# Performance work log

Measured on AMD Instinct MI355X. Metric: run time of the kernel, lower is better.

The kernel has to match this reference:

```python
import jax, jax.numpy as jnp
import numpy as np

S, B, V, E, H = 64, 32, 32000, 512, 1024


def gru_cell(x, h, Wih, Whh, bih, bhh):
    # PyTorch GRU cell math. x: [B, in], h: [B, H]
    gi = x @ Wih.T + bih          # [B, 3H]
    gh = h @ Whh.T + bhh          # [B, 3H]
    ir, iz, inn = jnp.split(gi, 3, axis=-1)
    hr, hz, hn = jnp.split(gh, 3, axis=-1)
    r = jax.nn.sigmoid(ir + hr)
    z = jax.nn.sigmoid(iz + hz)
    n = jnp.tanh(inn + r * hn)
    return (1.0 - z) * n + z * h


def run_gru(xs, h0, Wih, Whh, bih, bhh):
    def step(h, x):
        h = gru_cell(x, h, Wih, Whh, bih, bhh)
        return h, h
    _, hs = jax.lax.scan(step, h0, xs)
    return hs  # [S, B, H]


def setup_inputs():
    key = jax.random.key(0)
    ks = jax.random.split(key, 24)
    n = lambda k, shp, s=0.05: (jax.random.normal(k, shp, jnp.float32) * s)
    inp = {
        "input_seq": jax.random.randint(ks[0], (S, B), 0, V),
        "target_seq": jax.random.randint(ks[1], (S, B), 0, V),
        "emb": n(ks[2], (V, E)),
        # bidirectional encoder GRU (forward / backward directions)
        "enc_Wih_f": n(ks[3], (3 * H, E)), "enc_Whh_f": n(ks[4], (3 * H, H)),
        "enc_bih_f": n(ks[5], (3 * H,)),  "enc_bhh_f": n(ks[6], (3 * H,)),
        "enc_Wih_b": n(ks[7], (3 * H, E)), "enc_Whh_b": n(ks[8], (3 * H, H)),
        "enc_bih_b": n(ks[9], (3 * H,)),  "enc_bhh_b": n(ks[10], (3 * H,)),
        "encoder_init": n(ks[11], (2, H), 0.1),
        # decoder GRU: input = token(E) + glimpse(2H) + last_output(E)
        "dec_Wih": n(ks[12], (3 * H, 2 * E + 2 * H)), "dec_Whh": n(ks[13], (3 * H, H)),
        "dec_bih": n(ks[14], (3 * H,)), "dec_bhh": n(ks[15], (3 * H,)),
        "dec_init_h": n(ks[16], (H,), 0.1),
        "dec_init_out": n(ks[17], (E,), 0.1),
        "attn_W1": n(ks[18], (H, 3 * H)),  # Linear(3H -> H, bias=False)
        "attn_W2": n(ks[19], (1, H)),      # Linear(H -> 1, bias=False)
        "out_W": n(ks[20], (V, H)), "out_b": n(ks[21], (V,)),
    }
    return inp


def reference(input_seq, target_seq, emb,
              enc_Wih_f, enc_Whh_f, enc_bih_f, enc_bhh_f,
              enc_Wih_b, enc_Whh_b, enc_bih_b, enc_bhh_b, encoder_init,
              dec_Wih, dec_Whh, dec_bih, dec_bhh, dec_init_h, dec_init_out,
              attn_W1, attn_W2, out_W, out_b):
    x = emb[input_seq]            # [S, B, E]
    tgt = emb[target_seq]         # [S, B, E]
    bsz = x.shape[1]

    # bidirectional encoder
    h0f = jnp.broadcast_to(encoder_init[0], (bsz, H))
    h0b = jnp.broadcast_to(encoder_init[1], (bsz, H))
    fwd = run_gru(x, h0f, enc_Wih_f, enc_Whh_f, enc_bih_f, enc_bhh_f)
    bwd = run_gru(x[::-1], h0b, enc_Wih_b, enc_Whh_b, enc_bih_b, enc_bhh_b)[::-1]
    enc = jnp.concatenate([fwd, bwd], axis=-1)  # [S, B, 2H]

    def step(carry, inp_t):
        h, last_out = carry                      # [B,H], [B,E]
        tok, tg = inp_t                          # [B,E], [B,E]
        hexp = jnp.broadcast_to(h[None], (S, bsz, H))
        a = jnp.concatenate([enc, hexp], axis=-1)            # [S, B, 3H]
        scores = jnp.tanh(a @ attn_W1.T) @ attn_W2.T          # [S, B, 1]
        # NOTE: original uses nn.Softmax(dim=1) on [S,B,1] -> softmax over BATCH dim
        w = jax.nn.softmax(scores, axis=1)
        glimpse = (enc * w).sum(axis=0)                       # [B, 2H]
        dec_in = jnp.concatenate([tok, glimpse, last_out], axis=-1)
        h = gru_cell(dec_in, h, dec_Wih, dec_Whh, dec_bih, dec_bhh)
        probs = jax.nn.softmax(h @ out_W.T + out_b, axis=1)   # [B, V]
        return (h, tg), probs

    h0 = jnp.broadcast_to(dec_init_h, (bsz, H))
    o0 = jnp.broadcast_to(dec_init_out, (bsz, E))
    _, outs = jax.lax.scan(step, (h0, o0), (x, tgt))
    return outs  # [S, B, V]
```

## Files before the change

### kernel.cpp

```cpp
#include <hip/hip_runtime.h>
#include <hip/hip_bf16.h>

#define S_ 64
#define B_ 32
#define V_ 32000
#define E_ 512
#define H_ 1024
#define H3_ 3072

typedef __hip_bfloat16 bf16;
typedef __attribute__((ext_vector_type(8))) short s8v;
typedef __attribute__((ext_vector_type(4))) float f4;
typedef unsigned long long ull;

__device__ __forceinline__ float b2f(bf16 x){ return __bfloat162float(x); }
__device__ __forceinline__ bf16  f2b(float x){ return __float2bfloat16(x); }
__device__ __forceinline__ float bfu2f(unsigned short u){
  union { unsigned u; float f; } c; c.u = ((unsigned)u) << 16; return c.f;
}
#define MFMA16(a,b,c) __builtin_amdgcn_mfma_f32_16x16x32_bf16((a),(b),(c),0,0,0)

__device__ __forceinline__ float fsigmoid(float x){ return 1.f/(1.f + __expf(-x)); }
__device__ __forceinline__ float ftanh(float x){ float e2 = __expf(2.f*x); return 1.f - 2.f/(e2 + 1.f); }

__device__ __forceinline__ void gl16(const bf16* g, bf16* l){
  __builtin_amdgcn_global_load_lds((const __attribute__((address_space(1))) void*)g,
                                   (__attribute__((address_space(3))) void*)l, 16, 0, 0);
}

__device__ __forceinline__ void cast8(const float* __restrict__ s, bf16* __restrict__ d, int i){
  f4 a = *((const f4*)s + (size_t)i*2);
  f4 b = *((const f4*)s + (size_t)i*2 + 1);
  union { s8v v; bf16 h[8]; } o;
  #pragma unroll
  for (int k=0;k<4;k++){ o.h[k]=f2b(a[k]); o.h[4+k]=f2b(b[k]); }
  *((s8v*)d + i) = o.v;
}

__global__ __launch_bounds__(256) void prep_all_k(
  const float* __restrict__ emb, const int* __restrict__ iseq, const int* __restrict__ tseq,
  const float* __restrict__ dino,
  const float* __restrict__ wihf, const float* __restrict__ wihb,
  const float* __restrict__ whhf, const float* __restrict__ whhb,
  const float* __restrict__ whhd, const float* __restrict__ w1,
  const float* __restrict__ wihd, const float* __restrict__ outw,
  const float* __restrict__ einit, const float* __restrict__ bihf,
  const float* __restrict__ bihb, const float* __restrict__ dinh,
  bf16* __restrict__ x_b, bf16* __restrict__ lo_b,
  bf16* __restrict__ wihf_b, bf16* __restrict__ wihb_b,
  bf16* __restrict__ whhf_b, bf16* __restrict__ whhb_b,
  bf16* __restrict__ whhd_b, bf16* __restrict__ w1_b,
  bf16* __restrict__ wihd_b, bf16* __restrict__ outw_b,
  bf16* __restrict__ henc_b, float* __restrict__ hfE, float* __restrict__ bias_fb,
  bf16* __restrict__ hdb, float* __restrict__ hfD)
{
  const int task = blockIdx.y;
  const int stride = gridDim.x*256;
  const int i00 = blockIdx.x*256 + threadIdx.x;
  if (task < 8){
    const float* s; bf16* d; int n8;
    switch(task){
      case 0: s=wihf; d=wihf_b; n8=196608; break;
      case 1: s=wihb; d=wihb_b; n8=196608; break;
      case 2: s=whhf; d=whhf_b; n8=393216; break;
      case 3: s=whhb; d=whhb_b; n8=393216; break;
      case 4: s=whhd; d=whhd_b; n8=393216; break;
      case 5: s=w1;   d=w1_b;   n8=393216; break;
      case 6: s=wihd; d=wihd_b; n8=1179648; break;
      default: s=outw; d=outw_b; n8=4096000; break;
    }
    for (int i = i00; i < n8; i += stride) cast8(s, d, i);
  } else if (task == 8 || task == 9){
    for (int i = i00; i < 131072; i += stride){
      int row = i>>6, e8 = i&63;
      const float* src; bf16* d;
      if (task == 8){ src = emb + (size_t)iseq[row]*E_; d = x_b; }
      else {
        int t = row>>5, b = row&31;
        src = (t == 0) ? dino : (emb + (size_t)tseq[(t-1)*B_ + b]*E_);
        d = lo_b;
      }
      f4 a = *((const f4*)src + e8*2);
      f4 b = *((const f4*)src + e8*2 + 1);
      union { s8v v; bf16 h[8]; } o;
      #pragma unroll
      for (int k=0;k<4;k++){ o.h[k]=f2b(a[k]); o.h[4+k]=f2b(b[k]); }
      *((s8v*)d + i) = o.v;
    }
  } else if (task == 10){
    for (int i = i00; i < 8192; i += stride){
      int base = i*8;
      int dir = base>>15, rem = base&32767, col = rem&1023;
      const float* sp = einit + dir*H_ + col;
      f4 a = *(const f4*)sp, b = *(const f4*)(sp+4);
      union { s8v v; bf16 h[8]; } o;
      #pragma unroll
      for (int k=0;k<4;k++){ o.h[k]=f2b(a[k]); o.h[4+k]=f2b(b[k]); }
      *(s8v*)(henc_b + dir*32768 + rem) = o.v;
      *(f4*)(hfE + dir*32768 + rem) = a;
      *(f4*)(hfE + dir*32768 + rem + 4) = b;
      if (i < 6144) bias_fb[i] = (i < 3072) ? bihf[i] : bihb[i-3072];
    }
  } else {
    for (int i = i00; i < 4096; i += stride){
      int base = i*8;
      int col = base&1023;
      const float* sp = dinh + col;
      f4 a = *(const f4*)sp, b = *(const f4*)(sp+4);
      union { s8v v; bf16 h[8]; } o;
      #pragma unroll
      for (int k=0;k<4;k++){ o.h[k]=f2b(a[k]); o.h[4+k]=f2b(b[k]); }
      *(s8v*)(hdb + base) = o.v;
      *(f4*)(hfD + base) = a;
      *(f4*)(hfD + base + 4) = b;
    }
  }
}

template<int WB16>
__global__ __launch_bounds__(256) void gemm_bt(const bf16* __restrict__ A, int lda,
                                               const bf16* __restrict__ B, int ldb,
                                               const float* __restrict__ bias,
                                               void* __restrict__ Cp, int ldc, int K)
{
  __shared__ bf16 a_sm[128][32];
  __shared__ bf16 b_sm[128][32];
  const int tid = threadIdx.x;
  const int m0 = blockIdx.y*128, n0 = blockIdx.x*128;
  const int w = tid>>6, l = tid&63;
  const int wm = w>>1, wn = w&1;
  f4 acc[4][4];
  #pragma unroll
  for (int i=0;i<4;i++)
    #pragma unroll
    for (int j=0;j<4;j++) acc[i][j] = (f4){0.f,0.f,0.f,0.f};
  const int ar = l&15, koff = (l>>4)*8;
  const int glr = l>>2, gls = (l&3)*8;
  for (int k0 = 0; k0 < K; k0 += 32){
    __syncthreads();
    #pragma unroll
    for (int o = 0; o < 2; ++o){
      const int oo = w*2 + o;
      gl16(A + (size_t)(m0 + oo*16 + glr)*lda + k0 + gls, &a_sm[oo*16][0]);
      gl16(B + (size_t)(n0 + oo*16 + glr)*ldb + k0 + gls, &b_sm[oo*16][0]);
    }
    __syncthreads();
    s8v av[4], bv[4];
    #pragma unroll
    for (int i=0;i<4;i++) av[i] = *(const s8v*)&a_sm[wm*64 + i*16 + ar][koff];
    #pragma unroll
    for (int j=0;j<4;j++) bv[j] = *(const s8v*)&b_sm[wn*64 + j*16 + ar][koff];
    #pragma unroll
    for (int i=0;i<4;i++)
      #pragma unroll
      for (int j=0;j<4;j++)
        acc[i][j] = MFMA16(av[i], bv[j], acc[i][j]);
  }
  const int rb = (l>>4)*4;
  #pragma unroll
  for (int i=0;i<4;i++){
    #pragma unroll
    for (int j=0;j<4;j++){
      int col = n0 + wn*64 + j*16 + ar;
      float badd = bias ? bias[col] : 0.f;
      #pragma unroll
      for (int r=0;r<4;r++){
        int row = m0 + wm*64 + i*16 + rb + r;
        size_t idx = (size_t)row*ldc + col;
        float v = acc[i][j][r] + badd;
        if (WB16) ((bf16*)Cp)[idx] = f2b(v);
        else      ((float*)Cp)[idx] = v;
      }
    }
  }
}

__global__ __launch_bounds__(256) void gemm_dual(const bf16* __restrict__ A1, const bf16* __restrict__ A2,
                                                 const bf16* __restrict__ Bw, const float* __restrict__ bias,
                                                 float* __restrict__ C)
{
  __shared__ bf16 a_sm[128][32];
  __shared__ bf16 b_sm[128][32];
  const int tid = threadIdx.x;
  const int m0 = blockIdx.y*128, n0 = blockIdx.x*128;
  const int w = tid>>6, l = tid&63;
  const int wm = w>>1, wn = w&1;
  f4 acc[4][4];
  #pragma unroll
  for (int i=0;i<4;i++)
    #pragma unroll
    for (int j=0;j<4;j++) acc[i][j] = (f4){0.f,0.f,0.f,0.f};
  const int ar = l&15, koff = (l>>4)*8;
  const int glr = l>>2, gls = (l&3)*8;
  #pragma unroll 1
  for (int p = 0; p < 2; ++p){
    const bf16* Ax = p ? A2 : A1;
    const int cb = p ? 2560 : 0;
    for (int k0 = 0; k0 < 512; k0 += 32){
      __syncthreads();
      #pragma unroll
      for (int o = 0; o < 2; ++o){
        const int oo = w*2 + o;
        gl16(Ax + (size_t)(m0 + oo*16 + glr)*512 + k0 + gls, &a_sm[oo*16][0]);
        gl16(Bw + (size_t)(n0 + oo*16 + glr)*3072 + cb + k0 + gls, &b_sm[oo*16][0]);
      }
      __syncthreads();
      s8v av[4], bv[4];
      #pragma unroll
      for (int i=0;i<4;i++) av[i] = *(const s8v*)&a_sm[wm*64 + i*16 + ar][koff];
      #pragma unroll
      for (int j=0;j<4;j++) bv[j] = *(const s8v*)&b_sm[wn*64 + j*16 + ar][koff];
      #pragma unroll
      for (int i=0;i<4;i++)
        #pragma unroll
        for (int j=0;j<4;j++)
          acc[i][j] = MFMA16(av[i], bv[j], acc[i][j]);
    }
  }
  const int rb = (l>>4)*4;
  #pragma unroll
  for (int i=0;i<4;i++){
    #pragma unroll
    for (int j=0;j<4;j++){
      int col = n0 + wn*64 + j*16 + ar;
      float badd = bias[col];
      #pragma unroll
      for (int r=0;r<4;r++){
        int row = m0 + wm*64 + i*16 + rb + r;
        C[(size_t)row*H3_ + col] = acc[i][j][r] + badd;
      }
    }
  }
}

__global__ __launch_bounds__(256) void out_gemm_k(
  const bf16* __restrict__ A, const bf16* __restrict__ Bw,
  const float* __restrict__ bias, bf16* __restrict__ C)
{
  __shared__ bf16 a_sm[128][32];
  __shared__ bf16 b_sm[128][32];
  const int tid = threadIdx.x;
  const int bid = blockIdx.x;
  const int xcd = bid & 7, kk = bid >> 3;
  const int super = kk >> 6, rem = kk & 63;
  const int sm = super & 1, sn = super >> 1;
  const int mi = rem & 7, nj = rem >> 3;
  const int mt = sm*8 + mi, nl = sn*8 + nj;
  const int nt = nl*8 + xcd;
  if (nt >= 250) return;
  const int m0 = mt*128, n0 = nt*128;
  const int w = tid>>6, l = tid&63;
  const int wm = w>>1, wn = w&1;
  f4 acc[4][4];
  #pragma unroll
  for (int i=0;i<4;i++)
    #pragma unroll
    for (int j=0;j<4;j++) acc[i][j] = (f4){0.f,0.f,0.f,0.f};
  const int ar = l&15, koff = (l>>4)*8;
  const int glr = l>>2, gls = (l&3)*8;
  for (int k0 = 0; k0 < 1024; k0 += 32){
    __syncthreads();
    #pragma unroll
    for (int o = 0; o < 2; ++o){
      const int oo = w*2 + o;
      gl16(A + (size_t)(m0 + oo*16 + glr)*1024 + k0 + gls, &a_sm[oo*16][0]);
      gl16(Bw + (size_t)(n0 + oo*16 + glr)*1024 + k0 + gls, &b_sm[oo*16][0]);
    }
    __syncthreads();
    s8v av[4], bv[4];
    #pragma unroll
    for (int i=0;i<4;i++) av[i] = *(const s8v*)&a_sm[wm*64 + i*16 + ar][koff];
    #pragma unroll
    for (int j=0;j<4;j++) bv[j] = *(const s8v*)&b_sm[wn*64 + j*16 + ar][koff];
    #pragma unroll
    for (int i=0;i<4;i++)
      #pragma unroll
      for (int j=0;j<4;j++)
        acc[i][j] = MFMA16(av[i], bv[j], acc[i][j]);
  }
  const int rb = (l>>4)*4;
  float bj[4];
  #pragma unroll
  for (int j=0;j<4;j++) bj[j] = bias[n0 + wn*64 + j*16 + ar];
  #pragma unroll
  for (int i=0;i<4;i++){
    #pragma unroll
    for (int j=0;j<4;j++){
      const int col = n0 + wn*64 + j*16 + ar;
      #pragma unroll
      for (int r=0;r<4;r++){
        const int row = m0 + wm*64 + i*16 + rb + r;
        C[(size_t)row*V_ + col] = f2b(acc[i][j][r] + bj[j]);
      }
    }
  }
}

__global__ __launch_bounds__(256) void logit_stats_k(const bf16* __restrict__ lg,
                                                     float* __restrict__ rowM, float* __restrict__ rowL){
  __shared__ float wm[4], wl[4];
  const int tid = threadIdx.x;
  const bf16* p = lg + (size_t)blockIdx.x*V_;
  float m = -1e30f, lsum = 0.f;
  for (int c = tid; c < V_/8; c += 256){
    union { s8v v; unsigned short us[8]; } u;
    u.v = *((const s8v*)p + c);
    #pragma unroll
    for (int k = 0; k < 8; ++k){
      float v = bfu2f(u.us[k]);
      float mn = fmaxf(m, v);
      lsum = lsum*__expf(m - mn) + __expf(v - mn);
      m = mn;
    }
  }
  #pragma unroll
  for (int o = 32; o; o >>= 1){
    float mo = __shfl_xor(m, o), lo_ = __shfl_xor(lsum, o);
    float mn = fmaxf(m, mo);
    lsum = lsum*__expf(m - mn) + lo_*__expf(mo - mn);
    m = mn;
  }
  if ((tid&63)==0){ wm[tid>>6] = m; wl[tid>>6] = lsum; }
  __syncthreads();
  if (tid == 0){
    float M = fmaxf(fmaxf(wm[0],wm[1]), fmaxf(wm[2],wm[3]));
    float L = wl[0]*__expf(wm[0]-M) + wl[1]*__expf(wm[1]-M)
            + wl[2]*__expf(wm[2]-M) + wl[3]*__expf(wm[3]-M);
    rowM[blockIdx.x] = M;
    rowL[blockIdx.x] = L;
  }
}

__global__ __launch_bounds__(256) void norm_k(const bf16* __restrict__ lg,
                                              const float* __restrict__ rowM, const float* __restrict__ rowL,
                                              float* __restrict__ out){
  const int tid = threadIdx.x;
  const int row = blockIdx.x;
  const float M = rowM[row], inv = 1.f/rowL[row];
  const bf16* p = lg + (size_t)row*V_;
  float* q = out + (size_t)row*V_;
  for (int c = tid; c < V_/8; c += 256){
    union { s8v v; unsigned short us[8]; } u;
    u.v = *((const s8v*)p + c);
    f4 o0, o1;
    #pragma unroll
    for (int k = 0; k < 4; ++k) o0[k] = __expf(bfu2f(u.us[k]) - M)*inv;
    #pragma unroll
    for (int k = 0; k < 4; ++k) o1[k] = __expf(bfu2f(u.us[4+k]) - M)*inv;
    *((f4*)q + c*2)     = o0;
    *((f4*)q + c*2 + 1) = o1;
  }
}

__global__ __launch_bounds__(256) void enc_step_k(
  const float* __restrict__ gi_fb,
  const bf16* __restrict__ whhf, const bf16* __restrict__ whhb,
  const float* __restrict__ bhhf, const float* __restrict__ bhhb,
  const bf16* __restrict__ hrd_base, bf16* __restrict__ hwr_base,
  float* __restrict__ hfE, bf16* __restrict__ enc_out, int s)
{
  __shared__ bf16 hst[16][1032];
  __shared__ bf16 hsT[16][64];
  const int tid = threadIdx.x, bid = blockIdx.x;
  const int w = tid>>6, l = tid&63;
  const int lr = l&15, koff = (l>>4)*8, rb = (l>>4)*4;
  const int x = bid&7, g3 = bid>>3;
  const int dir = x>>2;
  const int mt = g3>>2;
  const int jtb = (x&3)*16 + (g3&3)*4;
  const int jt = jtb + w;
  const int col = jt*16 + lr;
  const bf16* W    = dir ? whhb : whhf;
  const float* bhh = dir ? bhhb : bhhf;
  const float br_ = bhh[col], bz_ = bhh[H_+col], bn_ = bhh[2*H_+col];
  const bf16* pr = W + (size_t)(jt*16 + lr)*H_ + koff;
  const bf16* pz = pr + (size_t)H_*H_;
  const bf16* pn = pz + (size_t)H_*H_;
  {
    const bf16* src = hrd_base + dir*32768 + (size_t)mt*16*H_;
    #pragma unroll
    for (int c = 0; c < 8; ++c){
      int g = c*256 + tid;
      int row = g>>7, off = g&127;
      *(s8v*)&hst[row][off*8] = *(const s8v*)(src + (size_t)row*H_ + off*8);
    }
  }
  __syncthreads();
  f4 accr = (f4){0,0,0,0}, accz = (f4){0,0,0,0}, accn = (f4){0,0,0,0};
  #pragma unroll 4
  for (int k0 = 0; k0 < H_; k0 += 32){
    s8v a = *(const s8v*)&hst[lr][koff + k0];
    accr = MFMA16(a, *(const s8v*)(pr + k0), accr);
    accz = MFMA16(a, *(const s8v*)(pz + k0), accz);
    accn = MFMA16(a, *(const s8v*)(pn + k0), accn);
  }
  const int es = dir ? (63 - s) : s;
  const int dcol = dir*3072 + col;
  #pragma unroll
  for (int ri = 0; ri < 4; ++ri){
    const int b_ = mt*16 + rb + ri;
    const size_t gr = (size_t)(es*B_ + b_)*6144;
    float ir = gi_fb[gr + dcol], iz = gi_fb[gr + 1024 + dcol], inn = gi_fb[gr + 2048 + dcol];
    float rg = fsigmoid(ir + accr[ri] + br_);
    float zg = fsigmoid(iz + accz[ri] + bz_);
    float ng = ftanh(inn + rg*(accn[ri] + bn_));
    float hold = hfE[dir*32768 + b_*H_ + col];
    float hnew = (1.f - zg)*ng + zg*hold;
    hfE[dir*32768 + b_*H_ + col] = hnew;
    hsT[rb+ri][w*16+lr] = f2b(hnew);
  }
  __syncthreads();
  {
    const int row = tid>>4, seg = tid&15;
    ull v = *(ull*)&hsT[row][seg*4];
    *(ull*)(hwr_base + dir*32768 + (size_t)(mt*16+row)*H_ + jtb*16 + seg*4) = v;
    *(ull*)(enc_out + (size_t)(es*B_ + mt*16+row)*2048 + dir*H_ + jtb*16 + seg*4) = v;
  }
}

__global__ __launch_bounds__(256) void dec_k1(
  const bf16* __restrict__ hd,
  const bf16* __restrict__ whhd, const float* __restrict__ bhhd,
  const bf16* __restrict__ w1b,
  float* __restrict__ gh, bf16* __restrict__ hW1b)
{
  __shared__ bf16 hst[16][1032];
  __shared__ float ghT[16][128];
  __shared__ bf16 hwT[16][128];
  const int tid = threadIdx.x, bid = blockIdx.x;
  const int w = tid>>6, l = tid&63;
  const int lr = l&15, koff = (l>>4)*8;
  const bool isP = bid < 16;
  const int hmt = isP ? (bid&1) : ((bid-16)&1);
  {
    const bf16* src = hd + (size_t)hmt*16*H_;
    #pragma unroll
    for (int c = 0; c < 8; ++c){
      int g = c*256 + tid;
      int row = g>>7, off = g&127;
      *(s8v*)&hst[row][off*8] = *(const s8v*)(src + (size_t)row*H_ + off*8);
    }
  }
  __syncthreads();
  if (isP){
    const int x2 = bid>>1;
    const int pjt0 = x2*8 + w*2;
    #pragma unroll
    for (int q = 0; q < 2; ++q){
      const bf16* pb = w1b + (size_t)((pjt0+q)*16 + lr)*H3_ + 2048 + koff;
      f4 acc = (f4){0,0,0,0};
      #pragma unroll 4
      for (int k0 = 0; k0 < H_; k0 += 32)
        acc = MFMA16(*(const s8v*)&hst[lr][koff+k0], *(const s8v*)(pb+k0), acc);
      #pragma unroll
      for (int r = 0; r < 4; ++r)
        hwT[(l>>4)*4+r][(w*2+q)*16 + lr] = f2b(acc[r]);
    }
    __syncthreads();
    #pragma unroll
    for (int i = 0; i < 2; ++i){
      int idx = tid + i*256;
      int row = idx>>5, seg = idx&31;
      *(ull*)(hW1b + (size_t)(hmt*16+row)*H_ + x2*128 + seg*4) = *(ull*)&hwT[row][seg*4];
    }
  } else {
    const int gb = bid - 16;
    const int rest = gb>>1;
    const int x3 = rest/3, gkk = rest%3;
    const int ntb = x3*24 + gkk*8;
    #pragma unroll
    for (int q = 0; q < 2; ++q){
      const int nt = ntb + w*2 + q;
      const bf16* pb = whhd + (size_t)(nt*16 + lr)*H_ + koff;
      const float bv = bhhd[nt*16 + lr];
      f4 acc = (f4){0,0,0,0};
      #pragma unroll 4
      for (int k0 = 0; k0 < H_; k0 += 32)
        acc = MFMA16(*(const s8v*)&hst[lr][koff+k0], *(const s8v*)(pb+k0), acc);
      #pragma unroll
      for (int r = 0; r < 4; ++r)
        ghT[(l>>4)*4+r][(w*2+q)*16 + lr] = acc[r] + bv;
    }
    __syncthreads();
    #pragma unroll
    for (int i = 0; i < 4; ++i){
      int idx = tid + i*256;
      int row = idx>>6, seg = idx&63;
      union{ float f[2]; ull u; } pk;
      pk.f[0] = ghT[row][seg*2]; pk.f[1] = ghT[row][seg*2+1];
      *(ull*)(gh + (size_t)(hmt*16+row)*H3_ + ntb*16 + seg*2) = pk.u;
    }
  }
}

__global__ __launch_bounds__(256) void dec_k2(
  const bf16* __restrict__ encW1b, const bf16* __restrict__ hW1b,
  const float* __restrict__ attnW2, float* __restrict__ wat)
{
  __shared__ float w2st[1024];
  __shared__ float scl[32];
  const int tid = threadIdx.x, s = blockIdx.x;
  w2st[tid] = attnW2[tid];
  w2st[tid+256] = attnW2[tid+256];
  w2st[tid+512] = attnW2[tid+512];
  w2st[tid+768] = attnW2[tid+768];
  __syncthreads();
  const int b = tid>>3, part = tid&7;
  const bf16* hp = hW1b + (size_t)b*H_ + part*128;
  const bf16* ep = encW1b + ((size_t)s*B_ + b)*H_ + part*128;
  const float* wp = w2st + part*128;
  float p = 0.f;
  #pragma unroll 4
  for (int ii = 0; ii < 16; ++ii){
    union { s8v v; unsigned short uu[8]; } hv, ev;
    hv.v = *(const s8v*)(hp + ii*8);
    ev.v = *(const s8v*)(ep + ii*8);
    #pragma unroll
    for (int k = 0; k < 8; ++k){
      float xx = bfu2f(ev.uu[k]) + bfu2f(hv.uu[k]);
      p += wp[ii*8+k]*ftanh(xx);
    }
  }
  p += __shfl_xor(p,1); p += __shfl_xor(p,2); p += __shfl_xor(p,4);
  if (part == 0) scl[b] = p;
  __syncthreads();
  if (tid < 32){
    float v = scl[tid];
    float m = v;
    #pragma unroll
    for (int o = 1; o <= 16; o <<= 1) m = fmaxf(m, __shfl_xor(m, o));
    float e = __expf(v - m);
    float Z = e;
    #pragma unroll
    for (int o = 1; o <= 16; o <<= 1) Z += __shfl_xor(Z, o);
    wat[s*B_ + tid] = e/Z;
  }
}

__global__ __launch_bounds__(256) void dec_k3(
  const float* __restrict__ gi_t,
  const bf16* __restrict__ encWgb, const float* __restrict__ gh,
  const float* __restrict__ wat,
  float* __restrict__ hfD, bf16* __restrict__ hd_w, bf16* __restrict__ hall_t)
{
  __shared__ float watst[64];
  __shared__ float part_[4][3][256];
  __shared__ bf16 hnewst[256];
  const int tid = threadIdx.x, bid = blockIdx.x;
  const int x = bid&7, g3 = bid>>3;
  const int db = 4*x + (g3&3), jq = g3>>2;
  const int jD = jq*256 + tid;
  if (tid < 64) watst[tid] = wat[tid*B_ + db];
  __syncthreads();
  const int lane = tid&63, wv = tid>>6;
  const int j0 = jq*256 + lane*4;
  f4 g0 = (f4){0,0,0,0}, g1 = (f4){0,0,0,0}, g2 = (f4){0,0,0,0};
  #pragma unroll 4
  for (int i = 0; i < 16; ++i){
    const int s2 = wv*16 + i;
    const float wt = watst[s2];
    const bf16* ro = encWgb + ((size_t)s2*B_ + db)*H3_;
    union{ ull u; unsigned short us[4]; } v0, v1, v2;
    v0.u = *(const ull*)(ro + j0);
    v1.u = *(const ull*)(ro + H_ + j0);
    v2.u = *(const ull*)(ro + 2*H_ + j0);
    #pragma unroll
    for (int k = 0; k < 4; ++k){
      g0[k] += wt*bfu2f(v0.us[k]);
      g1[k] += wt*bfu2f(v1.us[k]);
      g2[k] += wt*bfu2f(v2.us[k]);
    }
  }
  *(f4*)&part_[wv][0][lane*4] = g0;
  *(f4*)&part_[wv][1][lane*4] = g1;
  *(f4*)&part_[wv][2][lane*4] = g2;
  __syncthreads();
  float G0 = part_[0][0][tid]+part_[1][0][tid]+part_[2][0][tid]+part_[3][0][tid];
  float G1 = part_[0][1][tid]+part_[1][1][tid]+part_[2][1][tid]+part_[3][1][tid];
  float G2 = part_[0][2][tid]+part_[1][2][tid]+part_[2][2][tid]+part_[3][2][tid];
  const float* gp = gi_t + (size_t)db*H3_ + jD;
  float ir  = gp[0]    + G0;
  float iz  = gp[H_]   + G1;
  float inn = gp[2*H_] + G2;
  float hr_ = gh[(size_t)db*H3_ + jD];
  float hz_ = gh[(size_t)db*H3_ + H_ + jD];
  float hn_ = gh[(size_t)db*H3_ + 2*H_ + jD];
  float rg = fsigmoid(ir + hr_);
  float zg = fsigmoid(iz + hz_);
  float ng = ftanh(inn + rg*hn_);
  float hold = hfD[(size_t)db*H_ + jD];
  float hnew = (1.f - zg)*ng + zg*hold;
  hfD[(size_t)db*H_ + jD] = hnew;
  hnewst[tid] = f2b(hnew);
  __syncthreads();
  if (tid < 64){
    ull v = *(ull*)&hnewst[tid*4];
    *(ull*)(hd_w + (size_t)db*H_ + jq*256 + tid*4) = v;
    *(ull*)(hall_t + (size_t)db*H_ + jq*256 + tid*4) = v;
  }
}

extern "C" void kernel_launch(void* const* d_in, const int* in_sizes, int n_in,
                              void* d_out, int out_size, void* d_ws, size_t ws_size,
                              hipStream_t stream)
{
  (void)in_sizes; (void)n_in; (void)out_size; (void)ws_size;
  const int*   iseq  = (const int*)d_in[0];
  const int*   tseq  = (const int*)d_in[1];
  const float* emb   = (const float*)d_in[2];
  const float* wihf  = (const float*)d_in[3];
  const float* whhf_f= (const float*)d_in[4];
  const float* bihf  = (const float*)d_in[5];
  const float* bhhf  = (const float*)d_in[6];
  const float* wihb  = (const float*)d_in[7];
  const float* whhb_f= (const float*)d_in[8];
  const float* bihb  = (const float*)d_in[9];
  const float* bhhb  = (const float*)d_in[10];
  const float* einit = (const float*)d_in[11];
  const float* wihd  = (const float*)d_in[12];
  const float* whhd_f= (const float*)d_in[13];
  const float* bihd  = (const float*)d_in[14];
  const float* bhhd  = (const float*)d_in[15];
  const float* dinh  = (const float*)d_in[16];
  const float* dino  = (const float*)d_in[17];
  const float* w1    = (const float*)d_in[18];
  const float* w2    = (const float*)d_in[19];
  const float* outw  = (const float*)d_in[20];
  const float* outb  = (const float*)d_in[21];
  float* out = (float*)d_out;

  char* ws = (char*)d_ws;
  size_t off = 0;
  auto alloc = [&](size_t bytes)->char*{ char* p = ws + off; off += (bytes + 255) & ~(size_t)255; return p; };
  bf16* logits_b = (bf16*)ws;
  bf16* x_b      = (bf16*)alloc((size_t)2048*512*2);
  bf16* lo_b     = (bf16*)alloc((size_t)2048*512*2);
  bf16* wihf_b   = (bf16*)alloc((size_t)3072*512*2);
  bf16* wihb_b   = (bf16*)alloc((size_t)3072*512*2);
  bf16* whhf_b   = (bf16*)alloc((size_t)3072*1024*2);
  bf16* whhb_b   = (bf16*)alloc((size_t)3072*1024*2);
  bf16* wihd_b   = (bf16*)alloc((size_t)3072*3072*2);
  bf16* whhd_b   = (bf16*)alloc((size_t)3072*1024*2);
  bf16* w1_b     = (bf16*)alloc((size_t)1024*3072*2);
  float* gi_fb   = (float*)alloc((size_t)2048*6144*4);
  float* gi_d    = (float*)alloc((size_t)2048*3072*4);
  bf16* enc_b    = (bf16*)alloc((size_t)2048*2048*2);
  bf16* encW1_b  = (bf16*)alloc((size_t)2048*1024*2);
  bf16* encWg_b  = (bf16*)alloc((size_t)2048*3072*2);
  float* bias_fb = (float*)alloc((size_t)6144*4);
  bf16*  henc_b  = (bf16*)alloc((size_t)2*65536*2);
  float* hfE     = (float*)alloc((size_t)2*32768*4);
  bf16*  hdb     = (bf16*)alloc((size_t)2*32768*2);
  float* hfD     = (float*)alloc((size_t)32768*4);
  bf16*  hW1b    = (bf16*)alloc((size_t)32768*2);
  float* ghb     = (float*)alloc((size_t)32*3072*4);
  float* wat     = (float*)alloc((size_t)64*32*4);
  float* rowM    = (float*)alloc((size_t)2048*4);
  float* rowL    = (float*)alloc((size_t)2048*4);
  bf16* outw_b   = (bf16*)alloc((size_t)32000*1024*2);
  bf16*  hall_b  = (bf16*)alloc((size_t)2048*1024*2);

  prep_all_k<<<dim3(512,12), 256, 0, stream>>>(
      emb, iseq, tseq, dino,
      wihf, wihb, whhf_f, whhb_f, whhd_f, w1, wihd, outw,
      einit, bihf, bihb, dinh,
      x_b, lo_b, wihf_b, wihb_b, whhf_b, whhb_b, whhd_b, w1_b, wihd_b, outw_b,
      henc_b, hfE, bias_fb, hdb, hfD);

  gemm_bt<0><<<dim3(48,16), 256, 0, stream>>>(x_b, 512, wihf_b, 512, bias_fb, gi_fb, 6144, 512);
  gemm_dual<<<dim3(24,16), 256, 0, stream>>>(x_b, lo_b, wihd_b, bihd, gi_d);

  for (int s = 0; s < 64; ++s){
    const bf16* hrd = henc_b + (size_t)(s&1)*65536;
    bf16*       hwr = henc_b + (size_t)((s+1)&1)*65536;
    enc_step_k<<<64, 256, 0, stream>>>(gi_fb, whhf_b, whhb_b, bhhf, bhhb,
                                       hrd, hwr, hfE, enc_b, s);
  }

  gemm_bt<1><<<dim3(8,16),  256, 0, stream>>>(enc_b, 2048, w1_b,       3072, nullptr, encW1_b, 1024, 2048);
  gemm_bt<1><<<dim3(24,16), 256, 0, stream>>>(enc_b, 2048, wihd_b+512, 3072, nullptr, encWg_b, 3072, 2048);

  for (int t = 0; t < 64; ++t){
    const bf16* hdr = hdb + (size_t)(t&1)*32768;
    bf16*       hdw = hdb + (size_t)((t+1)&1)*32768;
    dec_k1<<<64, 256, 0, stream>>>(hdr, whhd_b, bhhd, w1_b, ghb, hW1b);
    dec_k2<<<64, 256, 0, stream>>>(encW1_b, hW1b, w2, wat);
    dec_k3<<<128, 256, 0, stream>>>(gi_d + (size_t)t*B_*H3_, encWg_b, ghb, wat,
                                    hfD, hdw, hall_b + (size_t)t*B_*H_);
  }

  out_gemm_k<<<4096, 256, 0, stream>>>(hall_b, outw_b, outb, logits_b);
  logit_stats_k<<<2048, 256, 0, stream>>>(logits_b, rowM, rowL);
  norm_k<<<2048, 256, 0, stream>>>(logits_b, rowM, rowL, out);
}
```

Before: 3.083 ms.

## Fuse decoder step kernels into one persistent kernel with grid barriers

Replaces the 192 per-step decoder launches (dec_k1/dec_k2/dec_k3 across 64 timesteps) with a single persistent 128-block kernel that loops over timesteps. Stages are separated by a software grid barrier built on atomic flags. Shared state is exchanged through relaxed agent-scope atomic loads and stores, and the decoder hidden state is kept in registers instead of an fp32 global buffer. This removes kernel launch gaps and a global read/write per step. In exchange it relies on all 128 blocks being co-resident and adds spin-wait barrier latency.

```diff
diff --git a/kernel.cpp b/kernel.cpp
--- a/kernel.cpp
+++ b/kernel.cpp
@@ -26,6 +26,40 @@
 __device__ __forceinline__ void gl16(const bf16* g, bf16* l){
   __builtin_amdgcn_global_load_lds((const __attribute__((address_space(1))) void*)g,
                                    (__attribute__((address_space(3))) void*)l, 16, 0, 0);
+}
+
+__device__ __forceinline__ ull dld64(const void* p){
+  return __hip_atomic_load((const ull*)p, __ATOMIC_RELAXED, __HIP_MEMORY_SCOPE_AGENT);
+}
+__device__ __forceinline__ void dst64(void* p, ull v){
+  __hip_atomic_store((ull*)p, v, __ATOMIC_RELAXED, __HIP_MEMORY_SCOPE_AGENT);
+}
+__device__ __forceinline__ float dldf(const void* p){
+  unsigned u = __hip_atomic_load((const unsigned*)p, __ATOMIC_RELAXED, __HIP_MEMORY_SCOPE_AGENT);
+  union{unsigned u; float f;} c; c.u=u; return c.f;
+}
+__device__ __forceinline__ unsigned dldu(const unsigned* p){
+  return __hip_atomic_load(p, __ATOMIC_RELAXED, __HIP_MEMORY_SCOPE_AGENT);
+}
+__device__ __forceinline__ void dstu(unsigned* p, unsigned v){
+  __hip_atomic_store(p, v, __ATOMIC_RELAXED, __HIP_MEMORY_SCOPE_AGENT);
+}
+
+__device__ __forceinline__ void pbar(unsigned* bar, unsigned ep, int bid, int nblk){
+  __syncthreads();
+  if (bid == 0){
+    const int i = threadIdx.x;
+    if (i > 0 && i < nblk){
+      while (dldu(bar + i*32) < ep) __builtin_amdgcn_s_sleep(1);
+    }
+    __syncthreads();
+    if (i < nblk) dstu(bar + 4096 + i*32, ep);
+  } else if (threadIdx.x == 0){
+    dstu(bar + bid*32, ep);
+    while (dldu(bar + 4096 + bid*32) < ep) __builtin_amdgcn_s_sleep(1);
+  }
+  __syncthreads();
+  asm volatile("" ::: "memory");
 }
 
 __device__ __forceinline__ void cast8(const float* __restrict__ s, bf16* __restrict__ d, int i){
@@ -51,8 +85,7 @@
   bf16* __restrict__ whhf_b, bf16* __restrict__ whhb_b,
   bf16* __restrict__ whhd_b, bf16* __restrict__ w1_b,
   bf16* __restrict__ wihd_b, bf16* __restrict__ outw_b,
-  bf16* __restrict__ henc_b, float* __restrict__ hfE, float* __restrict__ bias_fb,
-  bf16* __restrict__ hdb, float* __restrict__ hfD)
+  bf16* __restrict__ henc_b, float* __restrict__ hfE, float* __restrict__ bias_fb)
 {
   const int task = blockIdx.y;
   const int stride = gridDim.x*256;
@@ -87,7 +120,7 @@
       for (int k=0;k<4;k++){ o.h[k]=f2b(a[k]); o.h[4+k]=f2b(b[k]); }
       *((s8v*)d + i) = o.v;
     }
-  } else if (task == 10){
+  } else {
     for (int i = i00; i < 8192; i += stride){
       int base = i*8;
       int dir = base>>15, rem = base&32767, col = rem&1023;
@@ -100,19 +133,6 @@
       *(f4*)(hfE + dir*32768 + rem) = a;
       *(f4*)(hfE + dir*32768 + rem + 4) = b;
       if (i < 6144) bias_fb[i] = (i < 3072) ? bihf[i] : bihb[i-3072];
-    }
-  } else {
-    for (int i = i00; i < 4096; i += stride){
-      int base = i*8;
-      int col = base&1023;
-      const float* sp = dinh + col;
-      f4 a = *(const f4*)sp, b = *(const f4*)(sp+4);
-      union { s8v v; bf16 h[8]; } o;
-      #pragma unroll
-      for (int k=0;k<4;k++){ o.h[k]=f2b(a[k]); o.h[4+k]=f2b(b[k]); }
-      *(s8v*)(hdb + base) = o.v;
-      *(f4*)(hfD + base) = a;
-      *(f4*)(hfD + base + 4) = b;
     }
   }
 }
@@ -418,185 +438,202 @@
   }
 }
 
-__global__ __launch_bounds__(256) void dec_k1(
-  const bf16* __restrict__ hd,
+__global__ __launch_bounds__(256) void dec_persist_k(
+  const float* __restrict__ gi_d,
+  const bf16* __restrict__ encW1b,
+  const bf16* __restrict__ encWgb,
   const bf16* __restrict__ whhd, const float* __restrict__ bhhd,
   const bf16* __restrict__ w1b,
-  float* __restrict__ gh, bf16* __restrict__ hW1b)
+  const float* __restrict__ attnW2,
+  const float* __restrict__ dinh,
+  bf16* __restrict__ hdb,
+  bf16* __restrict__ hW1b,
+  float* __restrict__ gh,
+  float* __restrict__ wat,
+  bf16* __restrict__ h_all,
+  unsigned* __restrict__ bar)
 {
   __shared__ bf16 hst[16][1032];
   __shared__ float ghT[16][128];
   __shared__ bf16 hwT[16][128];
+  __shared__ float w2st[1024];
+  __shared__ float scl[32];
+  __shared__ float watv[32];
+  __shared__ float watst[64];
+  __shared__ float part_[4][3][256];
+  __shared__ bf16 hnewst[256];
   const int tid = threadIdx.x, bid = blockIdx.x;
   const int w = tid>>6, l = tid&63;
   const int lr = l&15, koff = (l>>4)*8;
-  const bool isP = bid < 16;
-  const int hmt = isP ? (bid&1) : ((bid-16)&1);
-  {
-    const bf16* src = hd + (size_t)hmt*16*H_;
-    #pragma unroll
-    for (int c = 0; c < 8; ++c){
-      int g = c*256 + tid;
-      int row = g>>7, off = g&127;
-      *(s8v*)&hst[row][off*8] = *(const s8v*)(src + (size_t)row*H_ + off*8);
-    }
-  }
-  __syncthreads();
-  if (isP){
-    const int x2 = bid>>1;
-    const int pjt0 = x2*8 + w*2;
-    #pragma unroll
-    for (int q = 0; q < 2; ++q){
-      const bf16* pb = w1b + (size_t)((pjt0+q)*16 + lr)*H3_ + 2048 + koff;
-      f4 acc = (f4){0,0,0,0};
-      #pragma unroll 4
-      for (int k0 = 0; k0 < H_; k0 += 32)
-        acc = MFMA16(*(const s8v*)&hst[lr][koff+k0], *(const s8v*)(pb+k0), acc);
-      #pragma unroll
-      for (int r = 0; r < 4; ++r)
-        hwT[(l>>4)*4+r][(w*2+q)*16 + lr] = f2b(acc[r]);
-    }
-    __syncthreads();
-    #pragma unroll
-    for (int i = 0; i < 2; ++i){
-      int idx = tid + i*256;
-      int row = idx>>5, seg = idx&31;
-      *(ull*)(hW1b + (size_t)(hmt*16+row)*H_ + x2*128 + seg*4) = *(ull*)&hwT[row][seg*4];
-    }
-  } else {
-    const int gb = bid - 16;
-    const int rest = gb>>1;
-    const int x3 = rest/3, gkk = rest%3;
-    const int ntb = x3*24 + gkk*8;
-    #pragma unroll
-    for (int q = 0; q < 2; ++q){
-      const int nt = ntb + w*2 + q;
-      const bf16* pb = whhd + (size_t)(nt*16 + lr)*H_ + koff;
-      const float bv = bhhd[nt*16 + lr];
-      f4 acc = (f4){0,0,0,0};
-      #pragma unroll 4
-      for (int k0 = 0; k0 < H_; k0 += 32)
-        acc = MFMA16(*(const s8v*)&hst[lr][koff+k0], *(const s8v*)(pb+k0), acc);
-      #pragma unroll
-      for (int r = 0; r < 4; ++r)
-        ghT[(l>>4)*4+r][(w*2+q)*16 + lr] = acc[r] + bv;
-    }
-    __syncthreads();
-    #pragma unroll
-    for (int i = 0; i < 4; ++i){
-      int idx = tid + i*256;
-      int row = idx>>6, seg = idx&63;
-      union{ float f[2]; ull u; } pk;
-      pk.f[0] = ghT[row][seg*2]; pk.f[1] = ghT[row][seg*2+1];
-      *(ull*)(gh + (size_t)(hmt*16+row)*H3_ + ntb*16 + seg*2) = pk.u;
-    }
-  }
-}
-
-__global__ __launch_bounds__(256) void dec_k2(
-  const bf16* __restrict__ encW1b, const bf16* __restrict__ hW1b,
-  const float* __restrict__ attnW2, float* __restrict__ wat)
-{
-  __shared__ float w2st[1024];
-  __shared__ float scl[32];
-  const int tid = threadIdx.x, s = blockIdx.x;
+  const int x = bid&7, g3 = bid>>3;
+  const int db = 4*x + (g3&3), jq = g3>>2;
+  const int jD = jq*256 + tid;
   w2st[tid] = attnW2[tid];
   w2st[tid+256] = attnW2[tid+256];
   w2st[tid+512] = attnW2[tid+512];
   w2st[tid+768] = attnW2[tid+768];
+  float hreg = dinh[jD];
+  hnewst[tid] = f2b(hreg);
   __syncthreads();
-  const int b = tid>>3, part = tid&7;
-  const bf16* hp = hW1b + (size_t)b*H_ + part*128;
-  const bf16* ep = encW1b + ((size_t)s*B_ + b)*H_ + part*128;
-  const float* wp = w2st + part*128;
-  float p = 0.f;
-  #pragma unroll 4
-  for (int ii = 0; ii < 16; ++ii){
-    union { s8v v; unsigned short uu[8]; } hv, ev;
-    hv.v = *(const s8v*)(hp + ii*8);
-    ev.v = *(const s8v*)(ep + ii*8);
-    #pragma unroll
-    for (int k = 0; k < 8; ++k){
-      float xx = bfu2f(ev.uu[k]) + bfu2f(hv.uu[k]);
-      p += wp[ii*8+k]*ftanh(xx);
-    }
-  }
-  p += __shfl_xor(p,1); p += __shfl_xor(p,2); p += __shfl_xor(p,4);
-  if (part == 0) scl[b] = p;
-  __syncthreads();
-  if (tid < 32){
-    float v = scl[tid];
-    float m = v;
-    #pragma unroll
-    for (int o = 1; o <= 16; o <<= 1) m = fmaxf(m, __shfl_xor(m, o));
-    float e = __expf(v - m);
-    float Z = e;
-    #pragma unroll
-    for (int o = 1; o <= 16; o <<= 1) Z += __shfl_xor(Z, o);
-    wat[s*B_ + tid] = e/Z;
-  }
-}
-
-__global__ __launch_bounds__(256) void dec_k3(
-  const float* __restrict__ gi_t,
-  const bf16* __restrict__ encWgb, const float* __restrict__ gh,
-  const float* __restrict__ wat,
-  float* __restrict__ hfD, bf16* __restrict__ hd_w, bf16* __restrict__ hall_t)
-{
-  __shared__ float watst[64];
-  __shared__ float part_[4][3][256];
-  __shared__ bf16 hnewst[256];
-  const int tid = threadIdx.x, bid = blockIdx.x;
-  const int x = bid&7, g3 = bid>>3;
-  const int db = 4*x + (g3&3), jq = g3>>2;
-  const int jD = jq*256 + tid;
-  if (tid < 64) watst[tid] = wat[tid*B_ + db];
-  __syncthreads();
-  const int lane = tid&63, wv = tid>>6;
-  const int j0 = jq*256 + lane*4;
-  f4 g0 = (f4){0,0,0,0}, g1 = (f4){0,0,0,0}, g2 = (f4){0,0,0,0};
-  #pragma unroll 4
-  for (int i = 0; i < 16; ++i){
-    const int s2 = wv*16 + i;
-    const float wt = watst[s2];
-    const bf16* ro = encWgb + ((size_t)s2*B_ + db)*H3_;
-    union{ ull u; unsigned short us[4]; } v0, v1, v2;
-    v0.u = *(const ull*)(ro + j0);
-    v1.u = *(const ull*)(ro + H_ + j0);
-    v2.u = *(const ull*)(ro + 2*H_ + j0);
-    #pragma unroll
-    for (int k = 0; k < 4; ++k){
-      g0[k] += wt*bfu2f(v0.us[k]);
-      g1[k] += wt*bfu2f(v1.us[k]);
-      g2[k] += wt*bfu2f(v2.us[k]);
-    }
-  }
-  *(f4*)&part_[wv][0][lane*4] = g0;
-  *(f4*)&part_[wv][1][lane*4] = g1;
-  *(f4*)&part_[wv][2][lane*4] = g2;
-  __syncthreads();
-  float G0 = part_[0][0][tid]+part_[1][0][tid]+part_[2][0][tid]+part_[3][0][tid];
-  float G1 = part_[0][1][tid]+part_[1][1][tid]+part_[2][1][tid]+part_[3][1][tid];
-  float G2 = part_[0][2][tid]+part_[1][2][tid]+part_[2][2][tid]+part_[3][2][tid];
-  const float* gp = gi_t + (size_t)db*H3_ + jD;
-  float ir  = gp[0]    + G0;
-  float iz  = gp[H_]   + G1;
-  float inn = gp[2*H_] + G2;
-  float hr_ = gh[(size_t)db*H3_ + jD];
-  float hz_ = gh[(size_t)db*H3_ + H_ + jD];
-  float hn_ = gh[(size_t)db*H3_ + 2*H_ + jD];
-  float rg = fsigmoid(ir + hr_);
-  float zg = fsigmoid(iz + hz_);
-  float ng = ftanh(inn + rg*hn_);
-  float hold = hfD[(size_t)db*H_ + jD];
-  float hnew = (1.f - zg)*ng + zg*hold;
-  hfD[(size_t)db*H_ + jD] = hnew;
-  hnewst[tid] = f2b(hnew);
-  __syncthreads();
-  if (tid < 64){
-    ull v = *(ull*)&hnewst[tid*4];
-    *(ull*)(hd_w + (size_t)db*H_ + jq*256 + tid*4) = v;
-    *(ull*)(hall_t + (size_t)db*H_ + jq*256 + tid*4) = v;
+  if (tid < 64) dst64(hdb + (size_t)db*H_ + jq*256 + tid*4, *(ull*)&hnewst[tid*4]);
+  pbar(bar, 1u, bid, 128);
+  unsigned ep = 2u;
+  for (int t = 0; t < 64; ++t){
+    if (bid < 64){
+      const bool isP = bid < 16;
+      const int hmt = isP ? (bid&1) : ((bid-16)&1);
+      {
+        const bf16* src = hdb + (size_t)hmt*16*H_;
+        #pragma unroll
+        for (int c = 0; c < 16; ++c){
+          int g = c*256 + tid;
+          *(ull*)&hst[g>>8][(g&255)*4] = dld64(src + g*4);
+        }
+      }
+      __syncthreads();
+      if (isP){
+        const int x2 = bid>>1;
+        const int pjt0 = x2*8 + w*2;
+        #pragma unroll
+        for (int q = 0; q < 2; ++q){
+          const bf16* pb = w1b + (size_t)((pjt0+q)*16 + lr)*H3_ + 2048 + koff;
+          f4 acc = (f4){0,0,0,0};
+          #pragma unroll 4
+          for (int k0 = 0; k0 < H_; k0 += 32)
+            acc = MFMA16(*(const s8v*)&hst[lr][koff+k0], *(const s8v*)(pb+k0), acc);
+          #pragma unroll
+          for (int r = 0; r < 4; ++r)
+            hwT[(l>>4)*4+r][(w*2+q)*16 + lr] = f2b(acc[r]);
+        }
+        __syncthreads();
+        #pragma unroll
+        for (int i = 0; i < 2; ++i){
+          int idx = tid + i*256;
+          int row = idx>>5, seg = idx&31;
+          dst64(hW1b + (size_t)(hmt*16+row)*H_ + x2*128 + seg*4, *(ull*)&hwT[row][seg*4]);
+        }
+      } else {
+        const int gb = bid - 16;
+        const int rest = gb>>1;
+        const int x3 = rest/3, gkk = rest%3;
+        const int ntb = x3*24 + gkk*8;
+        #pragma unroll
+        for (int q = 0; q < 2; ++q){
+          const int nt = ntb + w*2 + q;
+          const bf16* pb = whhd + (size_t)(nt*16 + lr)*H_ + koff;
+          const float bv = bhhd[nt*16 + lr];
+          f4 acc = (f4){0,0,0,0};
+          #pragma unroll 4
+          for (int k0 = 0; k0 < H_; k0 += 32)
+            acc = MFMA16(*(const s8v*)&hst[lr][koff+k0], *(const s8v*)(pb+k0), acc);
+          #pragma unroll
+          for (int r = 0; r < 4; ++r)
+            ghT[(l>>4)*4+r][(w*2+q)*16 + lr] = acc[r] + bv;
+        }
+        __syncthreads();
+        #pragma unroll
+        for (int i = 0; i < 4; ++i){
+          int idx = tid + i*256;
+          int row = idx>>6, seg = idx&63;
+          union{ float f[2]; ull u; } pk;
+          pk.f[0] = ghT[row][seg*2]; pk.f[1] = ghT[row][seg*2+1];
+          dst64(gh + (size_t)(hmt*16+row)*H3_ + ntb*16 + seg*2, pk.u);
+        }
+      }
+    }
+    pbar(bar, ep++, bid, 128);
+    if (bid < 64){
+      const int s = bid;
+      const int b = tid>>3, part = tid&7;
+      const bf16* hp = hW1b + (size_t)b*H_ + part*128;
+      const bf16* epr = encW1b + ((size_t)s*B_ + b)*H_ + part*128;
+      const float* wp = w2st + part*128;
+      float p = 0.f;
+      #pragma unroll 4
+      for (int ii = 0; ii < 16; ++ii){
+        union { ull u2[2]; unsigned short uu[8]; } hv;
+        hv.u2[0] = dld64(hp + ii*8);
+        hv.u2[1] = dld64(hp + ii*8 + 4);
+        union { s8v v; unsigned short uu[8]; } ev;
+        ev.v = *(const s8v*)(epr + ii*8);
+        #pragma unroll
+        for (int k = 0; k < 8; ++k){
+          float xx = bfu2f(ev.uu[k]) + bfu2f(hv.uu[k]);
+          p += wp[ii*8+k]*ftanh(xx);
+        }
+      }
+      p += __shfl_xor(p,1); p += __shfl_xor(p,2); p += __shfl_xor(p,4);
+      if (part == 0) scl[b] = p;
+      __syncthreads();
+      if (tid < 32){
+        float v = scl[tid];
+        float m = v;
+        #pragma unroll
+        for (int o = 1; o <= 16; o <<= 1) m = fmaxf(m, __shfl_xor(m, o));
+        float e = __expf(v - m);
+        float Z = e;
+        #pragma unroll
+        for (int o = 1; o <= 16; o <<= 1) Z += __shfl_xor(Z, o);
+        watv[tid] = e/Z;
+      }
+      __syncthreads();
+      if (tid < 16){
+        union{ float f[2]; ull u; } pk;
+        pk.f[0] = watv[tid*2]; pk.f[1] = watv[tid*2+1];
+        dst64(wat + s*B_ + tid*2, pk.u);
+      }
+    }
+    pbar(bar, ep++, bid, 128);
+    {
+      if (tid < 64) watst[tid] = dldf(wat + tid*B_ + db);
+      float hr_ = dldf(gh + (size_t)db*H3_ + jD);
+      float hz_ = dldf(gh + (size_t)db*H3_ + H_ + jD);
+      float hn_ = dldf(gh + (size_t)db*H3_ + 2*H_ + jD);
+      __syncthreads();
+      const int lane = tid&63, wv = tid>>6;
+      const int j0 = jq*256 + lane*4;
+      f4 g0 = (f4){0,0,0,0}, g1 = (f4){0,0,0,0}, g2 = (f4){0,0,0,0};
+      #pragma unroll 4
+      for (int i = 0; i < 16; ++i){
+        const int s2 = wv*16 + i;
+        const float wt = watst[s2];
+        const bf16* ro = encWgb + ((size_t)s2*B_ + db)*H3_;
+        union{ ull u; unsigned short us[4]; } v0, v1, v2;
+        v0.u = *(const ull*)(ro + j0);
+        v1.u = *(const ull*)(ro + H_ + j0);
+        v2.u = *(const ull*)(ro + 2*H_ + j0);
+        #pragma unroll
+        for (int k = 0; k < 4; ++k){
+          g0[k] += wt*bfu2f(v0.us[k]);
+          g1[k] += wt*bfu2f(v1.us[k]);
+          g2[k] += wt*bfu2f(v2.us[k]);
+        }
+      }
+      *(f4*)&part_[wv][0][lane*4] = g0;
+      *(f4*)&part_[wv][1][lane*4] = g1;
+      *(f4*)&part_[wv][2][lane*4] = g2;
+      __syncthreads();
+      float G0 = part_[0][0][tid]+part_[1][0][tid]+part_[2][0][tid]+part_[3][0][tid];
+      float G1 = part_[0][1][tid]+part_[1][1][tid]+part_[2][1][tid]+part_[3][1][tid];
+      float G2 = part_[0][2][tid]+part_[1][2][tid]+part_[2][2][tid]+part_[3][2][tid];
+      const float* gp = gi_d + ((size_t)t*B_ + db)*H3_ + jD;
+      float ir  = gp[0]    + G0;
+      float iz  = gp[H_]   + G1;
+      float inn = gp[2*H_] + G2;
+      float rg = fsigmoid(ir + hr_);
+      float zg = fsigmoid(iz + hz_);
+      float ng = ftanh(inn + rg*hn_);
+      float hnew = (1.f - zg)*ng + zg*hreg;
+      hreg = hnew;
+      hnewst[tid] = f2b(hnew);
+      __syncthreads();
+      if (tid < 64){
+        ull v = *(ull*)&hnewst[tid*4];
+        dst64(hdb + (size_t)db*H_ + jq*256 + tid*4, v);
+        *(ull*)(h_all + ((size_t)t*B_ + db)*H_ + jq*256 + tid*4) = v;
+      }
+    }
+    pbar(bar, ep++, bid, 128);
   }
 }
 
@@ -650,22 +687,24 @@
   float* bias_fb = (float*)alloc((size_t)6144*4);
   bf16*  henc_b  = (bf16*)alloc((size_t)2*65536*2);
   float* hfE     = (float*)alloc((size_t)2*32768*4);
-  bf16*  hdb     = (bf16*)alloc((size_t)2*32768*2);
-  float* hfD     = (float*)alloc((size_t)32768*4);
+  bf16*  hdb     = (bf16*)alloc((size_t)32768*2);
   bf16*  hW1b    = (bf16*)alloc((size_t)32768*2);
   float* ghb     = (float*)alloc((size_t)32*3072*4);
   float* wat     = (float*)alloc((size_t)64*32*4);
+  unsigned* bar  = (unsigned*)alloc((size_t)32768);
   float* rowM    = (float*)alloc((size_t)2048*4);
   float* rowL    = (float*)alloc((size_t)2048*4);
   bf16* outw_b   = (bf16*)alloc((size_t)32000*1024*2);
   bf16*  hall_b  = (bf16*)alloc((size_t)2048*1024*2);
 
-  prep_all_k<<<dim3(512,12), 256, 0, stream>>>(
+  hipMemsetAsync(bar, 0, 32768, stream);
+
+  prep_all_k<<<dim3(512,11), 256, 0, stream>>>(
       emb, iseq, tseq, dino,
       wihf, wihb, whhf_f, whhb_f, whhd_f, w1, wihd, outw,
       einit, bihf, bihb, dinh,
       x_b, lo_b, wihf_b, wihb_b, whhf_b, whhb_b, whhd_b, w1_b, wihd_b, outw_b,
-      henc_b, hfE, bias_fb, hdb, hfD);
+      henc_b, hfE, bias_fb);
 
   gemm_bt<0><<<dim3(48,16), 256, 0, stream>>>(x_b, 512, wihf_b, 512, bias_fb, gi_fb, 6144, 512);
   gemm_dual<<<dim3(24,16), 256, 0, stream>>>(x_b, lo_b, wihd_b, bihd, gi_d);
@@ -680,14 +719,8 @@
   gemm_bt<1><<<dim3(8,16),  256, 0, stream>>>(enc_b, 2048, w1_b,       3072, nullptr, encW1_b, 1024, 2048);
   gemm_bt<1><<<dim3(24,16), 256, 0, stream>>>(enc_b, 2048, wihd_b+512, 3072, nullptr, encWg_b, 3072, 2048);
 
-  for (int t = 0; t < 64; ++t){
-    const bf16* hdr = hdb + (size_t)(t&1)*32768;
-    bf16*       hdw = hdb + (size_t)((t+1)&1)*32768;
-    dec_k1<<<64, 256, 0, stream>>>(hdr, whhd_b, bhhd, w1_b, ghb, hW1b);
-    dec_k2<<<64, 256, 0, stream>>>(encW1_b, hW1b, w2, wat);
-    dec_k3<<<128, 256, 0, stream>>>(gi_d + (size_t)t*B_*H3_, encWg_b, ghb, wat,
-                                    hfD, hdw, hall_b + (size_t)t*B_*H_);
-  }
+  dec_persist_k<<<128, 256, 0, stream>>>(gi_d, encW1_b, encWg_b, whhd_b, bhhd, w1_b, w2, dinh,
+                                         hdb, hW1b, ghb, wat, hall_b, bar);
 
   out_gemm_k<<<4096, 256, 0, stream>>>(hall_b, outw_b, outb, logits_b);
   logit_stats_k<<<2048, 256, 0, stream>>>(logits_b, rowM, rowL);
```

Result: slower. 3.343 ms (+8.4%).
